# Kernel optimization log

Hardware: AMD Instinct MI355X
Metric: run time of the kernel (lower is better)

## Reference

```python
import jax, jax.numpy as jnp
import numpy as np

BLOCK_LEN = 64


def segsum(x):
    """x: (..., T) -> (..., T, T) with segsum[i,j] = sum_{k=j+1..i} x[k] (lower-tri incl diag), -inf above."""
    T = x.shape[-1]
    xc = jnp.cumsum(x, axis=-1)
    seg = xc[..., :, None] - xc[..., None, :]
    mask = jnp.tril(jnp.ones((T, T), dtype=bool))
    return jnp.where(mask, seg, -jnp.inf)


def setup_inputs() -> dict:
    key = jax.random.key(0)
    kx, ka, kb, kc = jax.random.split(key, 4)
    b, s, h, p, n = 4, 4096, 32, 64, 64
    X = jax.random.normal(kx, (b, s, h), dtype=jnp.float32)  # placeholder to keep split order stable
    X = jax.random.normal(kx, (b, s, h, p), dtype=jnp.float32)
    # A must be negative for a stable SSM decay (exp of cumulative sums stays bounded)
    A = -jax.random.uniform(ka, (b, s, h), dtype=jnp.float32, minval=0.0, maxval=1.0)
    B = jax.random.normal(kb, (b, s, h, n), dtype=jnp.float32)
    C = jax.random.normal(kc, (b, s, h, n), dtype=jnp.float32)
    return {"X": X, "A": A, "B": B, "C": C}


def reference(X, A, B, C):
    blk = BLOCK_LEN
    b, s, h, p = X.shape
    n = B.shape[-1]
    c = s // blk
    # chunk: b (c l) ... -> b c l ...
    Xc = X.reshape(b, c, blk, h, p)
    Bc = B.reshape(b, c, blk, h, n)
    Cc = C.reshape(b, c, blk, h, n)
    Ac = A.reshape(b, c, blk, h).transpose(0, 3, 1, 2)  # b h c l
    A_cumsum = jnp.cumsum(Ac, axis=-1)                  # b h c l

    # 1. intra-chunk (diagonal block) output
    L = jnp.exp(segsum(Ac))                             # b h c l s
    Y_diag = jnp.einsum("bclhn,bcshn,bhcls,bcshp->bclhp", Cc, Bc, L, Xc)

    # 2. intra-chunk states (chunk-final state assuming zero initial state)
    decay_states = jnp.exp(A_cumsum[..., -1:] - A_cumsum)
    states = jnp.einsum("bclhn,bhcl,bclhp->bchpn", Bc, decay_states, Xc)

    # 3. inter-chunk recurrence over chunk boundaries
    init = jnp.zeros_like(states[:, :1])
    states = jnp.concatenate([init, states], axis=1)    # b (c+1) h p n
    A_last = jnp.pad(A_cumsum[..., -1], ((0, 0), (0, 0), (1, 0)))  # b h (c+1)
    decay_chunk = jnp.exp(segsum(A_last))               # b h (c+1) (c+1)
    new_states = jnp.einsum("bhzc,bchpn->bzhpn", decay_chunk, states)
    states_in = new_states[:, :-1]                      # state entering each chunk

    # 4. state -> output
    state_decay_out = jnp.exp(A_cumsum)
    Y_off = jnp.einsum("bclhn,bchpn,bhcl->bclhp", Cc, states_in, state_decay_out)

    Y = (Y_diag + Y_off).reshape(b, s, h, p)
    return Y
```

## Files before the change

### kernel.cpp

```cpp
#include <hip/hip_runtime.h>

namespace {

typedef __attribute__((ext_vector_type(8))) short short8;
typedef __attribute__((ext_vector_type(4))) float f32x4;

constexpr int Hh = 32, Ssq = 4096, NCH = 64;
constexpr int GR = 2048;
constexpr int ST = 68;

__device__ inline unsigned short f2bf(float f) {
  unsigned u = __float_as_uint(f);
  u += 0x7FFFu + ((u >> 16) & 1u);
  return (unsigned short)(u >> 16);
}
__device__ inline float bf2f(unsigned short s) {
  return __uint_as_float(((unsigned)s) << 16);
}

__device__ inline short8 frag(const unsigned short* p) {
  union { short8 s; uint2 u[2]; } r;
  r.u[0] = *(const uint2*)p;
  r.u[1] = *(const uint2*)(p + 4);
  return r.s;
}

__global__ __launch_bounds__(256, 4)
void k1a_chunkstate(const float* __restrict__ X0, const float* __restrict__ A0,
                    const float* __restrict__ B0, unsigned short* __restrict__ S16) {
  __shared__ unsigned short BTs[64 * ST];
  __shared__ unsigned short XTs[64 * ST];
  __shared__ float ielb[64];
  __shared__ float eab;

  const int tid = threadIdx.x;
  const int hi = blockIdx.x & 31, ci = (blockIdx.x >> 5) & 63, bi = blockIdx.x >> 11;
  if (ci == 63) return;

  const float* Xg = X0 + (((size_t)bi * Ssq + ci * 64) * Hh + hi) * 64;
  const float* Bg = B0 + (((size_t)bi * Ssq + ci * 64) * Hh + hi) * 64;
  const float* Ag = A0 + ((size_t)bi * Ssq + ci * 64) * Hh + hi;
  unsigned short* sp = S16 + ((size_t)(bi * Hh + hi) * NCH + ci) * 4096;

  const int w = tid >> 6, lane = tid & 63, lr = lane & 15, lk = lane >> 4;

  if (tid < 64) {
    float a = Ag[(size_t)tid * Hh];
#pragma unroll
    for (int off = 1; off < 64; off <<= 1) {
      float v = __shfl_up(a, off);
      if (tid >= off) a += v;
    }
    ielb[tid] = __expf(-a);
    if (tid == 63) eab = __expf(a);
  }
  __syncthreads();

  {
    const int r = tid >> 2, cb = (tid & 3) * 4;
    const float iel = ielb[r];
    const float* bp = Bg + (size_t)r * GR;
    const float* xp = Xg + (size_t)r * GR;
#pragma unroll
    for (int j = 0; j < 4; ++j) {
      const int c = cb + 16 * j;
      float4 bv = *(const float4*)(bp + c);
      BTs[(c + 0) * ST + r] = f2bf(bv.x * iel);
      BTs[(c + 1) * ST + r] = f2bf(bv.y * iel);
      BTs[(c + 2) * ST + r] = f2bf(bv.z * iel);
      BTs[(c + 3) * ST + r] = f2bf(bv.w * iel);
      float4 xv = *(const float4*)(xp + c);
      XTs[(c + 0) * ST + r] = f2bf(xv.x);
      XTs[(c + 1) * ST + r] = f2bf(xv.y);
      XTs[(c + 2) * ST + r] = f2bf(xv.z);
      XTs[(c + 3) * ST + r] = f2bf(xv.w);
    }
  }
  __syncthreads();

  const float ea = eab;
#pragma unroll
  for (int tp = 0; tp < 4; ++tp) {
    f32x4 acc = {0.f, 0.f, 0.f, 0.f};
#pragma unroll
    for (int ks = 0; ks < 2; ++ks)
      acc = __builtin_amdgcn_mfma_f32_16x16x32_bf16(
          frag(&XTs[(tp * 16 + lr) * ST + ks * 32 + lk * 8]),
          frag(&BTs[(w * 16 + lr) * ST + ks * 32 + lk * 8]), acc, 0, 0, 0);
#pragma unroll
    for (int i = 0; i < 4; ++i)
      sp[(tp * 16 + lk * 4 + i) * 64 + w * 16 + lr] = f2bf(acc[i] * ea);
  }
}

__global__ __launch_bounds__(256)
void k1b_scan(const float* __restrict__ A0, unsigned short* __restrict__ S16) {
  __shared__ float part[256];
  __shared__ float eat[64];

  const int tid = threadIdx.x;
  const int sl8 = blockIdx.x & 7, hi = (blockIdx.x >> 3) & 31, bi = blockIdx.x >> 8;
  const float* Ag = A0 + (size_t)bi * Ssq * Hh + hi;

  {
    const int c = tid >> 2, q = tid & 3;
    float s = 0.f;
#pragma unroll
    for (int k = 0; k < 16; ++k) s += Ag[(size_t)(c * 64 + q * 16 + k) * Hh];
    part[tid] = s;
  }
  __syncthreads();
  if (tid < 64)
    eat[tid] = __expf(part[tid * 4] + part[tid * 4 + 1] + part[tid * 4 + 2] + part[tid * 4 + 3]);
  __syncthreads();

  unsigned short* base =
      S16 + (size_t)(bi * Hh + hi) * NCH * 4096 + sl8 * 512 + tid * 2;
  float s0 = 0.f, s1 = 0.f;
  unsigned cur = *(const unsigned*)base;
  for (int c = 0; c < 63; ++c) {
    unsigned nxt = 0u;
    if (c + 1 < 63) nxt = *(const unsigned*)(base + (size_t)(c + 1) * 4096);
    const float ea = eat[c];
    s0 = s0 * ea + bf2f((unsigned short)(cur & 0xffffu));
    s1 = s1 * ea + bf2f((unsigned short)(cur >> 16));
    *(unsigned*)(base + (size_t)(c + 1) * 4096) =
        (unsigned)f2bf(s0) | ((unsigned)f2bf(s1) << 16);
    cur = nxt;
  }
}

__global__ __launch_bounds__(256, 4)
void k2_y(const float* __restrict__ X0, const float* __restrict__ A0,
          const float* __restrict__ B0, const float* __restrict__ C0,
          const unsigned short* __restrict__ S16, float* __restrict__ Y0) {
  __shared__ unsigned short Cs[64 * ST];
  __shared__ unsigned short Bsh[64 * ST];
  __shared__ unsigned short XT[64 * ST];
  __shared__ unsigned short Sb[64 * ST];
  __shared__ unsigned short Gs[64 * ST];
  __shared__ float elb[64], ielb2[64];

  const int tid = threadIdx.x;
  const int hi = blockIdx.x & 31, ci = (blockIdx.x >> 5) & 63, bi = blockIdx.x >> 11;

  const float* Xg = X0 + (((size_t)bi * Ssq + ci * 64) * Hh + hi) * 64;
  const float* Bg = B0 + (((size_t)bi * Ssq + ci * 64) * Hh + hi) * 64;
  const float* Cg = C0 + (((size_t)bi * Ssq + ci * 64) * Hh + hi) * 64;
  const float* Ag = A0 + ((size_t)bi * Ssq + ci * 64) * Hh + hi;
  const unsigned short* Sg = S16 + ((size_t)(bi * Hh + hi) * NCH + ci) * 4096;
  float* Yg = Y0 + (((size_t)bi * Ssq + ci * 64) * Hh + hi) * 64;

  const int w = tid >> 6, lane = tid & 63, lr = lane & 15, lk = lane >> 4;

  for (int i = tid; i < 64 * ST; i += 256) Gs[i] = 0;

  if (tid < 64) {
    float a = Ag[(size_t)tid * Hh];
#pragma unroll
    for (int off = 1; off < 64; off <<= 1) {
      float v = __shfl_up(a, off);
      if (tid >= off) a += v;
    }
    elb[tid] = __expf(a);
    ielb2[tid] = __expf(-a);
  }
  __syncthreads();

  {
    const int r = tid >> 2, cb = (tid & 3) * 4;
    const float iel = ielb2[r];
    const float* bp = Bg + (size_t)r * GR;
    const float* cp = Cg + (size_t)r * GR;
    const float* xp = Xg + (size_t)r * GR;
#pragma unroll
    for (int j = 0; j < 4; ++j) {
      const int c = cb + 16 * j;
      float4 bv = *(const float4*)(bp + c);
      float4 cv = *(const float4*)(cp + c);
      unsigned short bb[4] = {f2bf(bv.x * iel), f2bf(bv.y * iel),
                              f2bf(bv.z * iel), f2bf(bv.w * iel)};
      unsigned short cc[4] = {f2bf(cv.x), f2bf(cv.y), f2bf(cv.z), f2bf(cv.w)};
      *(uint2*)&Bsh[r * ST + c] = *(const uint2*)bb;
      *(uint2*)&Cs[r * ST + c] = *(const uint2*)cc;
      float4 xv = *(const float4*)(xp + c);
      XT[(c + 0) * ST + r] = f2bf(xv.x);
      XT[(c + 1) * ST + r] = f2bf(xv.y);
      XT[(c + 2) * ST + r] = f2bf(xv.z);
      XT[(c + 3) * ST + r] = f2bf(xv.w);
    }
    if (ci == 0) {
#pragma unroll
      for (int j = 0; j < 4; ++j) {
        const int q = tid + j * 256;
        uint2 z = {0u, 0u};
        *(uint2*)&Sb[(q >> 4) * ST + (q & 15) * 4] = z;
      }
    } else {
#pragma unroll
      for (int j = 0; j < 4; ++j) {
        const int q = tid + j * 256;
        *(uint2*)&Sb[(q >> 4) * ST + (q & 15) * 4] = *(const uint2*)(Sg + q * 4);
      }
    }
  }
  __syncthreads();

  {
    int tl[3] = {-1, -1, -1}, ts[3] = {0, 0, 0};
    switch (w) {
      case 0: tl[0] = 0; ts[0] = 0; tl[1] = 1; ts[1] = 0; tl[2] = 1; ts[2] = 1; break;
      case 1: tl[0] = 2; ts[0] = 0; tl[1] = 2; ts[1] = 1; tl[2] = 2; ts[2] = 2; break;
      case 2: tl[0] = 3; ts[0] = 0; tl[1] = 3; ts[1] = 1; break;
      case 3: tl[0] = 3; ts[0] = 2; tl[1] = 3; ts[1] = 3; break;
    }
#pragma unroll
    for (int t = 0; t < 3; ++t) {
      if (tl[t] >= 0) {
        f32x4 acc = {0.f, 0.f, 0.f, 0.f};
#pragma unroll
        for (int ks = 0; ks < 2; ++ks)
          acc = __builtin_amdgcn_mfma_f32_16x16x32_bf16(
              frag(&Cs[(tl[t] * 16 + lr) * ST + ks * 32 + lk * 8]),
              frag(&Bsh[(ts[t] * 16 + lr) * ST + ks * 32 + lk * 8]), acc, 0, 0, 0);
        const int gcol = ts[t] * 16 + lr;
#pragma unroll
        for (int i = 0; i < 4; ++i) {
          const int grow = tl[t] * 16 + lk * 4 + i;
          float gv = (gcol <= grow) ? acc[i] * elb[grow] : 0.f;
          Gs[grow * ST + gcol] = f2bf(gv);
        }
      }
    }
  }
  __syncthreads();

  {
#pragma unroll
    for (int tp = 0; tp < 4; ++tp) {
      f32x4 aD = {0.f, 0.f, 0.f, 0.f}, aO = {0.f, 0.f, 0.f, 0.f};
#pragma unroll
      for (int ks = 0; ks < 2; ++ks) {
        const int ko = ks * 32 + lk * 8;
        aD = __builtin_amdgcn_mfma_f32_16x16x32_bf16(
            frag(&Gs[(w * 16 + lr) * ST + ko]), frag(&XT[(tp * 16 + lr) * ST + ko]), aD, 0, 0, 0);
        aO = __builtin_amdgcn_mfma_f32_16x16x32_bf16(
            frag(&Cs[(w * 16 + lr) * ST + ko]), frag(&Sb[(tp * 16 + lr) * ST + ko]), aO, 0, 0, 0);
      }
#pragma unroll
      for (int i = 0; i < 4; ++i) {
        const int row = w * 16 + lk * 4 + i;
        Yg[(size_t)row * GR + tp * 16 + lr] = aD[i] + elb[row] * aO[i];
      }
    }
  }
}

}

extern "C" void kernel_launch(void* const* d_in, const int* in_sizes, int n_in,
                              void* d_out, int out_size, void* d_ws, size_t ws_size,
                              hipStream_t stream) {
  const float* X = (const float*)d_in[0];
  const float* A = (const float*)d_in[1];
  const float* B = (const float*)d_in[2];
  const float* C = (const float*)d_in[3];
  float* Y = (float*)d_out;
  unsigned short* S16 = (unsigned short*)d_ws;
  (void)in_sizes; (void)n_in; (void)out_size; (void)ws_size;
  k1a_chunkstate<<<dim3(8192), dim3(256), 0, stream>>>(X, A, B, S16);
  k1b_scan<<<dim3(1024), dim3(256), 0, stream>>>(A, S16);
  k2_y<<<dim3(8192), dim3(256), 0, stream>>>(X, A, B, C, S16, Y);
}
```

Before: 244.5 us.

## Reuse B shared buffer for decay matrix, unroll state scan, raise k1a occupancy

The y kernel drops its separate Gs shared buffer. It computes the C·Bᵀ tiles into registers, syncs, then writes the masked, decayed G tile back over Bsh, explicitly zeroing only the upper-triangular 16x16 tiles. This cuts shared memory per block, which can allow more resident blocks, and removes the full Gs zeroing loop, at the cost of an extra barrier. Separately, the chunk-state scan keeps four loads in flight to hide global latency, and the chunk-state kernel's launch bounds hint rises to 8 blocks, which may cause register pressure.

```diff
diff --git a/kernel.cpp b/kernel.cpp
--- a/kernel.cpp
+++ b/kernel.cpp
@@ -25,7 +25,7 @@
   return r.s;
 }
 
-__global__ __launch_bounds__(256, 4)
+__global__ __launch_bounds__(256, 8)
 void k1a_chunkstate(const float* __restrict__ X0, const float* __restrict__ A0,
                     const float* __restrict__ B0, unsigned short* __restrict__ S16) {
   __shared__ unsigned short BTs[64 * ST];
@@ -117,17 +117,26 @@
   unsigned short* base =
       S16 + (size_t)(bi * Hh + hi) * NCH * 4096 + sl8 * 512 + tid * 2;
   float s0 = 0.f, s1 = 0.f;
-  unsigned cur = *(const unsigned*)base;
-  for (int c = 0; c < 63; ++c) {
-    unsigned nxt = 0u;
-    if (c + 1 < 63) nxt = *(const unsigned*)(base + (size_t)(c + 1) * 4096);
+
+  auto L = [&](int c) -> unsigned {
+    return (c < 63) ? *(const unsigned*)(base + (size_t)c * 4096) : 0u;
+  };
+  auto step = [&](int c, unsigned v) {
     const float ea = eat[c];
-    s0 = s0 * ea + bf2f((unsigned short)(cur & 0xffffu));
-    s1 = s1 * ea + bf2f((unsigned short)(cur >> 16));
+    s0 = s0 * ea + bf2f((unsigned short)(v & 0xffffu));
+    s1 = s1 * ea + bf2f((unsigned short)(v >> 16));
     *(unsigned*)(base + (size_t)(c + 1) * 4096) =
         (unsigned)f2bf(s0) | ((unsigned)f2bf(s1) << 16);
-    cur = nxt;
-  }
+  };
+
+  unsigned q0 = L(0), q1 = L(1), q2 = L(2), q3 = L(3);
+  for (int c = 0; c < 60; c += 4) {
+    step(c + 0, q0); q0 = L(c + 4);
+    step(c + 1, q1); q1 = L(c + 5);
+    step(c + 2, q2); q2 = L(c + 6);
+    step(c + 3, q3); q3 = L(c + 7);
+  }
+  step(60, q0); step(61, q1); step(62, q2);
 }
 
 __global__ __launch_bounds__(256, 4)
@@ -138,7 +147,6 @@
   __shared__ unsigned short Bsh[64 * ST];
   __shared__ unsigned short XT[64 * ST];
   __shared__ unsigned short Sb[64 * ST];
-  __shared__ unsigned short Gs[64 * ST];
   __shared__ float elb[64], ielb2[64];
 
   const int tid = threadIdx.x;
@@ -152,8 +160,6 @@
   float* Yg = Y0 + (((size_t)bi * Ssq + ci * 64) * Hh + hi) * 64;
 
   const int w = tid >> 6, lane = tid & 63, lr = lane & 15, lk = lane >> 4;
-
-  for (int i = tid; i < 64 * ST; i += 256) Gs[i] = 0;
 
   if (tid < 64) {
     float a = Ag[(size_t)tid * Hh];
@@ -206,32 +212,51 @@
   }
   __syncthreads();
 
-  {
-    int tl[3] = {-1, -1, -1}, ts[3] = {0, 0, 0};
-    switch (w) {
-      case 0: tl[0] = 0; ts[0] = 0; tl[1] = 1; ts[1] = 0; tl[2] = 1; ts[2] = 1; break;
-      case 1: tl[0] = 2; ts[0] = 0; tl[1] = 2; ts[1] = 1; tl[2] = 2; ts[2] = 2; break;
-      case 2: tl[0] = 3; ts[0] = 0; tl[1] = 3; ts[1] = 1; break;
-      case 3: tl[0] = 3; ts[0] = 2; tl[1] = 3; ts[1] = 3; break;
-    }
+  int tl[3] = {-1, -1, -1}, ts[3] = {0, 0, 0};
+  int zr[2] = {-1, -1}, zc[2] = {0, 0};
+  switch (w) {
+    case 0: tl[0] = 0; ts[0] = 0; tl[1] = 1; ts[1] = 0; tl[2] = 1; ts[2] = 1;
+            zr[0] = 0; zc[0] = 1; zr[1] = 0; zc[1] = 2; break;
+    case 1: tl[0] = 2; ts[0] = 0; tl[1] = 2; ts[1] = 1; tl[2] = 2; ts[2] = 2;
+            zr[0] = 0; zc[0] = 3; break;
+    case 2: tl[0] = 3; ts[0] = 0; tl[1] = 3; ts[1] = 1;
+            zr[0] = 1; zc[0] = 2; zr[1] = 1; zc[1] = 3; break;
+    case 3: tl[0] = 3; ts[0] = 2; tl[1] = 3; ts[1] = 3;
+            zr[0] = 2; zc[0] = 3; break;
+  }
+  f32x4 ga[3];
+#pragma unroll
+  for (int t = 0; t < 3; ++t) {
+    ga[t] = (f32x4){0.f, 0.f, 0.f, 0.f};
+    if (tl[t] >= 0) {
+#pragma unroll
+      for (int ks = 0; ks < 2; ++ks)
+        ga[t] = __builtin_amdgcn_mfma_f32_16x16x32_bf16(
+            frag(&Cs[(tl[t] * 16 + lr) * ST + ks * 32 + lk * 8]),
+            frag(&Bsh[(ts[t] * 16 + lr) * ST + ks * 32 + lk * 8]), ga[t], 0, 0, 0);
+    }
+  }
+  __syncthreads();
+
+  {
 #pragma unroll
     for (int t = 0; t < 3; ++t) {
       if (tl[t] >= 0) {
-        f32x4 acc = {0.f, 0.f, 0.f, 0.f};
-#pragma unroll
-        for (int ks = 0; ks < 2; ++ks)
-          acc = __builtin_amdgcn_mfma_f32_16x16x32_bf16(
-              frag(&Cs[(tl[t] * 16 + lr) * ST + ks * 32 + lk * 8]),
-              frag(&Bsh[(ts[t] * 16 + lr) * ST + ks * 32 + lk * 8]), acc, 0, 0, 0);
         const int gcol = ts[t] * 16 + lr;
 #pragma unroll
         for (int i = 0; i < 4; ++i) {
           const int grow = tl[t] * 16 + lk * 4 + i;
-          float gv = (gcol <= grow) ? acc[i] * elb[grow] : 0.f;
-          Gs[grow * ST + gcol] = f2bf(gv);
+          float gv = (gcol <= grow) ? ga[t][i] * elb[grow] : 0.f;
+          Bsh[grow * ST + gcol] = f2bf(gv);
         }
       }
     }
+    const int zrow = lane >> 2, zq = lane & 3;
+    uint2 z = {0u, 0u};
+#pragma unroll
+    for (int t = 0; t < 2; ++t)
+      if (zr[t] >= 0)
+        *(uint2*)&Bsh[(zr[t] * 16 + zrow) * ST + zc[t] * 16 + zq * 4] = z;
   }
   __syncthreads();
 
@@ -243,7 +268,7 @@
       for (int ks = 0; ks < 2; ++ks) {
         const int ko = ks * 32 + lk * 8;
         aD = __builtin_amdgcn_mfma_f32_16x16x32_bf16(
-            frag(&Gs[(w * 16 + lr) * ST + ko]), frag(&XT[(tp * 16 + lr) * ST + ko]), aD, 0, 0, 0);
+            frag(&Bsh[(w * 16 + lr) * ST + ko]), frag(&XT[(tp * 16 + lr) * ST + ko]), aD, 0, 0, 0);
         aO = __builtin_amdgcn_mfma_f32_16x16x32_bf16(
             frag(&Cs[(w * 16 + lr) * ST + ko]), frag(&Sb[(tp * 16 + lr) * ST + ko]), aO, 0, 0, 0);
       }
```

Result: no change. 241.4 us (-1.2%).
